# Optimization experiments

Measured on AMD Instinct MI355X. Metric: run time of the kernel, lower is better.

The kernel has to match this reference:

```python
import jax, jax.numpy as jnp
import numpy as np

DIM, H, KV, HD, WIN = 1024, 16, 4, 64, 512
EPS = 1e-6


def rmsnorm(x, w, eps=EPS):
    # torch.nn.RMSNorm: x * rsqrt(mean(x^2, -1) + eps) * w
    return x * jax.lax.rsqrt(jnp.mean(x * x, axis=-1, keepdims=True) + eps) * w


def setup_inputs() -> dict:
    key = jax.random.key(0)
    ks = jax.random.split(key, 7)
    B, T = 4, 2048
    s = 0.02
    return {
        "x": jax.random.normal(ks[0], (B, T, DIM), dtype=jnp.float32),
        "wq": jax.random.normal(ks[1], (H * HD, DIM), dtype=jnp.float32) * s,
        "wk": jax.random.normal(ks[2], (KV * HD, DIM), dtype=jnp.float32) * s,
        "wv": jax.random.normal(ks[3], (KV * HD, DIM), dtype=jnp.float32) * s,
        "wo": jax.random.normal(ks[4], (DIM, H * HD), dtype=jnp.float32) * s,
        "q_norm_w": jnp.ones((HD,), dtype=jnp.float32),
        "k_norm_w": jnp.ones((HD,), dtype=jnp.float32),
    }


def reference(x, wq, wk, wv, wo, q_norm_w, k_norm_w):
    B, T, D = x.shape
    rep = H // KV
    q = (x @ wq.T).reshape(B, T, H, HD)
    k = (x @ wk.T).reshape(B, T, KV, HD)
    v = (x @ wv.T).reshape(B, T, KV, HD)
    q = rmsnorm(q, q_norm_w)
    k = rmsnorm(k, k_norm_w)
    # GQA repeat: each kv head repeated `rep` times contiguously
    k = jnp.repeat(k, rep, axis=2)  # [B,T,H,HD]
    v = jnp.repeat(v, rep, axis=2)
    # scores [B,H,T,T]
    scores = jnp.einsum('bqhd,bkhd->bhqk', q, k) / jnp.sqrt(jnp.float32(HD))
    i = jnp.arange(T)[:, None]
    j = jnp.arange(T)[None, :]
    mask = (i >= j) & (i - j < WIN)  # causal sliding window band
    scores = jnp.where(mask, scores, -jnp.inf)
    attn = jax.nn.softmax(scores, axis=-1)
    y = jnp.einsum('bhqk,bkhd->bqhd', attn, v).reshape(B, T, H * HD)
    return y @ wo.T
```

## Files before the change

### kernel.cpp

```cpp
#include <hip/hip_runtime.h>
#include <hip/hip_bf16.h>

#define DIMD 1024
#define NH   16
#define NKV  4
#define HDIM 64
#define WINSZ 512
#define BB   4
#define TT   2048
#define MROWS (BB*TT)
#define NQKV 1536

typedef __attribute__((ext_vector_type(8))) short short8;
typedef __attribute__((ext_vector_type(4))) float f32x4;

static __device__ __forceinline__ short f2bf(float f) {
  __hip_bfloat16 h = __float2bfloat16(f);
  return __builtin_bit_cast(short, h);
}
static __device__ __forceinline__ float bf2f(short s) {
  return __bfloat162float(__builtin_bit_cast(__hip_bfloat16, s));
}
static __device__ __forceinline__ unsigned pk2(float a, float b) {
  unsigned lo = (unsigned short)f2bf(a);
  unsigned hi = (unsigned short)f2bf(b);
  return lo | (hi << 16);
}

static __device__ __forceinline__ void gld_lds16(const void* g, void* l) {
  __builtin_amdgcn_global_load_lds(
      (const __attribute__((address_space(1))) unsigned int*)g,
      (__attribute__((address_space(3))) unsigned int*)l, 16, 0, 0);
}

template<int N>
static __device__ __forceinline__ float dpp_ror(float x) {
  return __builtin_bit_cast(float, __builtin_amdgcn_update_dpp(
      0, __builtin_bit_cast(int, x), 0x120 + N, 0xF, 0xF, true));
}

__global__ __launch_bounds__(256) void cvt_all_kernel(
    const float* __restrict__ x, const float* __restrict__ wq,
    const float* __restrict__ wk, const float* __restrict__ wv,
    const float* __restrict__ wo,
    short* __restrict__ xb, short* __restrict__ wqkvb, short* __restrict__ wob) {
  size_t u = (size_t)blockIdx.x * 256 + threadIdx.x;
  const float* src; short* dst;
  if (u < 2097152)                   { src = x;  dst = xb; }
  else if ((u -= 2097152) < 262144)  { src = wq; dst = wqkvb; }
  else if ((u -= 262144) < 65536)    { src = wk; dst = wqkvb + 1024*1024; }
  else if ((u -= 65536) < 65536)     { src = wv; dst = wqkvb + 1280*1024; }
  else { u -= 65536;                   src = wo; dst = wob; }
  float4 v = ((const float4*)src)[u];
  short4 o;
  o.x = f2bf(v.x); o.y = f2bf(v.y); o.z = f2bf(v.z); o.w = f2bf(v.w);
  ((short4*)dst)[u] = o;
}

#define BMT 128
#define BNT 128
#define BKT 64

template<bool OUT_BF16>
__global__ __launch_bounds__(256) void gemm_bt(
    const short* __restrict__ A, const short* __restrict__ Bw,
    void* __restrict__ Cout, int M, int N, int K) {
  __shared__ __align__(16) short As[BMT*BKT];
  __shared__ __align__(16) short Bs[BNT*BKT];

  int nwg  = gridDim.x;
  int orig = blockIdx.x;
  int wg   = (orig & 7) * (nwg >> 3) + (orig >> 3);
  int tiles_n = N / BNT;
  int m0 = (wg / tiles_n) * BMT;
  int n0 = (wg % tiles_n) * BNT;

  int tid = threadIdx.x;
  int lane = tid & 63, wv = tid >> 6;
  int l15 = lane & 15, lg = lane >> 4;
  int wr = wv >> 1, wc = wv & 1;

  f32x4 acc[4][4] = {};

  for (int k0 = 0; k0 < K; k0 += BKT) {
    __syncthreads();
    const char* Abase = (const char*)(A + (size_t)m0 * K + k0);
    const char* Bbase = (const char*)(Bw + (size_t)n0 * K + k0);
#pragma unroll
    for (int i = 0; i < 4; ++i) {
      int idx = i * 256 + tid;
      int row = idx >> 3;
      int cb  = (idx & 7) << 4;
      int scb = cb ^ ((row & 7) << 4);
      gld_lds16(Abase + (size_t)row * (K * 2) + scb,
                (char*)As + ((i * 256 + wv * 64) << 4));
      gld_lds16(Bbase + (size_t)row * (K * 2) + scb,
                (char*)Bs + ((i * 256 + wv * 64) << 4));
    }
    __syncthreads();

#pragma unroll
    for (int kk = 0; kk < 2; ++kk) {
      short8 af[4], bfr[4];
      int kb = (kk * 32 + lg * 8) * 2;
#pragma unroll
      for (int mi = 0; mi < 4; ++mi) {
        int row = wr * 64 + mi * 16 + l15;
        af[mi] = *(const short8*)((const char*)As + row * 128 + (kb ^ ((row & 7) << 4)));
      }
#pragma unroll
      for (int ni = 0; ni < 4; ++ni) {
        int row = wc * 64 + ni * 16 + l15;
        bfr[ni] = *(const short8*)((const char*)Bs + row * 128 + (kb ^ ((row & 7) << 4)));
      }
#pragma unroll
      for (int mi = 0; mi < 4; ++mi)
#pragma unroll
        for (int ni = 0; ni < 4; ++ni)
          acc[mi][ni] = __builtin_amdgcn_mfma_f32_16x16x32_bf16(af[mi], bfr[ni], acc[mi][ni], 0, 0, 0);
    }
  }

  int crow0 = m0 + wr * 64, ccol0 = n0 + wc * 64;
#pragma unroll
  for (int mi = 0; mi < 4; ++mi)
#pragma unroll
    for (int ni = 0; ni < 4; ++ni)
#pragma unroll
      for (int r = 0; r < 4; ++r) {
        int row = crow0 + mi * 16 + lg * 4 + r;
        int col = ccol0 + ni * 16 + l15;
        float v = acc[mi][ni][r];
        if (OUT_BF16) ((short*)Cout)[(size_t)row * N + col] = f2bf(v);
        else          ((float*)Cout)[(size_t)row * N + col] = v;
      }
}

__global__ __launch_bounds__(256) void qk_norm_kernel(
    const short* __restrict__ qkv, const float* __restrict__ qw,
    const float* __restrict__ kw, short* __restrict__ Qh, short* __restrict__ Kh) {
  unsigned gid = blockIdx.x * 16u + (threadIdx.x >> 4);
  int l = threadIdx.x & 15;
  unsigned row = gid / 20u;
  int s = (int)(gid - row * 20u);
  int b = row >> 11, t = row & 2047;
  bool isq = s < 16;
  int col = isq ? s * 64 : 1024 + (s - 16) * 64;
  const short* rp = qkv + (size_t)row * NQKV + col + l * 4;
  short4 v4 = *(const short4*)rp;
  float f0 = bf2f(v4.x), f1 = bf2f(v4.y), f2 = bf2f(v4.z), f3 = bf2f(v4.w);
  float ss = f0 * f0 + f1 * f1 + f2 * f2 + f3 * f3;
  ss += dpp_ror<1>(ss); ss += dpp_ror<2>(ss);
  ss += dpp_ror<4>(ss); ss += dpp_ror<8>(ss);
  float r = rsqrtf(ss * (1.0f / 64.0f) + 1e-6f);
  float4 w4 = *(const float4*)((isq ? qw : kw) + l * 4);
  short4 o;
  o.x = f2bf(f0 * r * w4.x); o.y = f2bf(f1 * r * w4.y);
  o.z = f2bf(f2 * r * w4.z); o.w = f2bf(f3 * r * w4.w);
  if (isq) *(short4*)(Qh + (((size_t)b * NH + s) * TT + t) * HDIM + l * 4) = o;
  else     *(short4*)(Kh + (((size_t)b * NKV + (s - 16)) * TT + t) * HDIM + l * 4) = o;
}

__global__ __launch_bounds__(256) void vtrans_kernel(
    const short* __restrict__ qkv, short* __restrict__ Vt) {
  int tb = blockIdx.x, kv = blockIdx.y, b = blockIdx.z;
  __shared__ short tile[64][72];
  int tid = threadIdx.x;
#pragma unroll
  for (int i = 0; i < 2; ++i) {
    int idx = i * 256 + tid;
    int tr = idx >> 3;
    int c8 = (idx & 7) * 8;
    int t = tb * 64 + tr;
    const short* src = qkv + (size_t)(b * TT + t) * NQKV + 1280 + kv * 64 + c8;
    short8 v = *(const short8*)src;
#pragma unroll
    for (int j = 0; j < 8; ++j) tile[tr][c8 + j] = v[j];
  }
  __syncthreads();
#pragma unroll
  for (int i = 0; i < 2; ++i) {
    int idx = i * 256 + tid;
    int d = idx >> 3;
    int t8 = (idx & 7) * 8;
    short8 o;
#pragma unroll
    for (int j = 0; j < 8; ++j) o[j] = tile[t8 + j][d];
    short* dst = Vt + (((size_t)(b * NKV + kv) * HDIM) + d) * TT + tb * 64 + t8;
    *(short8*)dst = o;
  }
}

#define C1A 0.180336880f
#define C2A 11.5415603f

__global__ __launch_bounds__(128) void attn_kernel(
    const short* __restrict__ Qh, const short* __restrict__ Kh,
    const short* __restrict__ Vt, short* __restrict__ Y) {
  int wgid = blockIdx.x;
  int qh = wgid >> 6;
  int hb = wgid & 63;
  int h = hb >> 2, b = hb & 3;
  int tid = threadIdx.x, lane = tid & 63;
  int khalf = tid >> 6;
  int l15 = lane & 15, lg = lane >> 4;
  int kvh = h >> 2;
  int q0 = qh * 32;
  const short* Qp = Qh + (((size_t)b * NH + h) * TT + q0) * HDIM;
  const short* Kp = Kh + ((size_t)b * NKV + kvh) * TT * HDIM;
  const short* Vp = Vt + ((size_t)b * NKV + kvh) * HDIM * TT;

  short8 aqA0 = *(const short8*)(Qp + l15 * HDIM + lg * 8);
  short8 aqA1 = *(const short8*)(Qp + l15 * HDIM + 32 + lg * 8);
  short8 aqB0 = *(const short8*)(Qp + (16 + l15) * HDIM + lg * 8);
  short8 aqB1 = *(const short8*)(Qp + (16 + l15) * HDIM + 32 + lg * 8);

  float lpA = 0.f, lpB = 0.f;
  f32x4 yA[4] = {}, yB[4] = {};

  __shared__ __align__(16) char smem[9216];
  short* PA = (short*)smem + khalf * 2304;
  short* PB = PA + 1152;

  int lo = q0 - (WINSZ - 1); if (lo < 0) lo = 0;
  int klo = lo & ~63;
  int nt = (q0 + 32 - klo + 63) >> 6;
  int tmid = (nt + 1) >> 1;
  int t0 = khalf ? tmid : 0;
  int t1 = khalf ? nt : tmid;

  int qiA = q0 + l15, qiB = qiA + 16;

  for (int t = t0; t < t1; ++t) {
    int kc = klo + t * 64;
    short8 bk0[4], bk1[4], bv0[4], bv1[4];
#pragma unroll
    for (int nc = 0; nc < 4; ++nc) {
      const short* kb = Kp + (size_t)(kc + nc * 16 + l15) * HDIM + lg * 8;
      bk0[nc] = *(const short8*)kb;
      bk1[nc] = *(const short8*)(kb + 32);
    }
#pragma unroll
    for (int dt = 0; dt < 4; ++dt) {
      const short* vb = Vp + (size_t)(dt * 16 + l15) * TT + kc + lg * 8;
      bv0[dt] = *(const short8*)vb;
      bv1[dt] = *(const short8*)(vb + 32);
    }
    f32x4 sA[4], sB[4];
#pragma unroll
    for (int nc = 0; nc < 4; ++nc) {
      f32x4 zA = {}, zB = {};
      zA = __builtin_amdgcn_mfma_f32_16x16x32_bf16(bk0[nc], aqA0, zA, 0, 0, 0);
      zB = __builtin_amdgcn_mfma_f32_16x16x32_bf16(bk0[nc], aqB0, zB, 0, 0, 0);
      zA = __builtin_amdgcn_mfma_f32_16x16x32_bf16(bk1[nc], aqA1, zA, 0, 0, 0);
      zB = __builtin_amdgcn_mfma_f32_16x16x32_bf16(bk1[nc], aqB1, zB, 0, 0, 0);
      sA[nc] = zA; sB[nc] = zB;
    }
    bool intA = (kc >= q0 - 496) && (kc + 63 <= q0);
    bool intB = (kc >= q0 - 480) && (kc + 63 <= q0 + 16);
    if (intA && intB) {
#pragma unroll
      for (int nc = 0; nc < 4; ++nc) {
        float pa0 = __builtin_amdgcn_exp2f(fmaf(sA[nc][0], C1A, -C2A));
        float pa1 = __builtin_amdgcn_exp2f(fmaf(sA[nc][1], C1A, -C2A));
        float pa2 = __builtin_amdgcn_exp2f(fmaf(sA[nc][2], C1A, -C2A));
        float pa3 = __builtin_amdgcn_exp2f(fmaf(sA[nc][3], C1A, -C2A));
        float pb0 = __builtin_amdgcn_exp2f(fmaf(sB[nc][0], C1A, -C2A));
        float pb1 = __builtin_amdgcn_exp2f(fmaf(sB[nc][1], C1A, -C2A));
        float pb2 = __builtin_amdgcn_exp2f(fmaf(sB[nc][2], C1A, -C2A));
        float pb3 = __builtin_amdgcn_exp2f(fmaf(sB[nc][3], C1A, -C2A));
        lpA += (pa0 + pa1) + (pa2 + pa3);
        lpB += (pb0 + pb1) + (pb2 + pb3);
        *(uint2*)(PA + l15 * 72 + nc * 16 + lg * 4) = uint2{pk2(pa0, pa1), pk2(pa2, pa3)};
        *(uint2*)(PB + l15 * 72 + nc * 16 + lg * 4) = uint2{pk2(pb0, pb1), pk2(pb2, pb3)};
      }
    } else {
      int kjb = kc + lg * 4;
#pragma unroll
      for (int nc = 0; nc < 4; ++nc) {
        float pa[4], pb[4];
#pragma unroll
        for (int r = 0; r < 4; ++r) {
          int kj = kjb + nc * 16 + r;
          bool okA = (kj <= qiA) && (qiA - kj < WINSZ);
          bool okB = (kj <= qiB) && (qiB - kj < WINSZ);
          pa[r] = okA ? __builtin_amdgcn_exp2f(fmaf(sA[nc][r], C1A, -C2A)) : 0.f;
          pb[r] = okB ? __builtin_amdgcn_exp2f(fmaf(sB[nc][r], C1A, -C2A)) : 0.f;
        }
        lpA += (pa[0] + pa[1]) + (pa[2] + pa[3]);
        lpB += (pb[0] + pb[1]) + (pb[2] + pb[3]);
        *(uint2*)(PA + l15 * 72 + nc * 16 + lg * 4) = uint2{pk2(pa[0], pa[1]), pk2(pa[2], pa[3])};
        *(uint2*)(PB + l15 * 72 + nc * 16 + lg * 4) = uint2{pk2(pb[0], pb[1]), pk2(pb[2], pb[3])};
      }
    }
    short8 apA0 = *(const short8*)(PA + l15 * 72 + lg * 8);
    short8 apA1 = *(const short8*)(PA + l15 * 72 + 32 + lg * 8);
    short8 apB0 = *(const short8*)(PB + l15 * 72 + lg * 8);
    short8 apB1 = *(const short8*)(PB + l15 * 72 + 32 + lg * 8);
#pragma unroll
    for (int dt = 0; dt < 4; ++dt) {
      yA[dt] = __builtin_amdgcn_mfma_f32_16x16x32_bf16(apA0, bv0[dt], yA[dt], 0, 0, 0);
      yB[dt] = __builtin_amdgcn_mfma_f32_16x16x32_bf16(apB0, bv0[dt], yB[dt], 0, 0, 0);
      yA[dt] = __builtin_amdgcn_mfma_f32_16x16x32_bf16(apA1, bv1[dt], yA[dt], 0, 0, 0);
      yB[dt] = __builtin_amdgcn_mfma_f32_16x16x32_bf16(apB1, bv1[dt], yB[dt], 0, 0, 0);
    }
  }

  lpA += __shfl_xor(lpA, 16); lpA += __shfl_xor(lpA, 32);
  lpB += __shfl_xor(lpB, 16); lpB += __shfl_xor(lpB, 32);

  __syncthreads();
  f32x4* ybuf = (f32x4*)smem;
  float* lbufA = (float*)(smem + 8192);
  float* lbufB = lbufA + 16;
  if (khalf) {
#pragma unroll
    for (int dt = 0; dt < 4; ++dt) {
      ybuf[dt * 64 + lane] = yA[dt];
      ybuf[(4 + dt) * 64 + lane] = yB[dt];
    }
    if (lg == 0) { lbufA[l15] = lpA; lbufB[l15] = lpB; }
  }
  __syncthreads();
  if (!khalf) {
#pragma unroll
    for (int dt = 0; dt < 4; ++dt) {
      f32x4 pa = ybuf[dt * 64 + lane];
      f32x4 pb = ybuf[(4 + dt) * 64 + lane];
#pragma unroll
      for (int r = 0; r < 4; ++r) { yA[dt][r] += pa[r]; yB[dt][r] += pb[r]; }
    }
    float invqA = 1.0f / (lpA + lbufA[l15]);
    float invqB = 1.0f / (lpB + lbufB[l15]);
#pragma unroll
    for (int r = 0; r < 4; ++r) {
      float invA = __builtin_bit_cast(float, __builtin_amdgcn_ds_bpermute(
          (lg * 4 + r) << 2, __builtin_bit_cast(int, invqA)));
      float invB = __builtin_bit_cast(float, __builtin_amdgcn_ds_bpermute(
          (lg * 4 + r) << 2, __builtin_bit_cast(int, invqB)));
      int qiAo = q0 + lg * 4 + r, qiBo = qiAo + 16;
#pragma unroll
      for (int dt = 0; dt < 4; ++dt) {
        Y[((size_t)(b * TT + qiAo)) * DIMD + h * HDIM + dt * 16 + l15] = f2bf(yA[dt][r] * invA);
        Y[((size_t)(b * TT + qiBo)) * DIMD + h * HDIM + dt * 16 + l15] = f2bf(yB[dt][r] * invB);
      }
    }
  }
}

extern "C" void kernel_launch(void* const* d_in, const int* in_sizes, int n_in,
                              void* d_out, int out_size, void* d_ws, size_t ws_size,
                              hipStream_t stream) {
  const float* x  = (const float*)d_in[0];
  const float* wq = (const float*)d_in[1];
  const float* wk = (const float*)d_in[2];
  const float* wv = (const float*)d_in[3];
  const float* wo = (const float*)d_in[4];
  const float* qw = (const float*)d_in[5];
  const float* kw = (const float*)d_in[6];

  char* ws = (char*)d_ws;
  short* xb    = (short*)(ws + 0);
  short* wqkvb = (short*)(ws + 16777216);
  short* wob   = (short*)(ws + 19922944);
  short* qkv   = (short*)(ws + 22020096);
  short* Qh    = (short*)(ws + 47185920);
  short* Kh    = (short*)(ws + 63963136);
  short* Vt    = (short*)(ws + 68157440);
  short* Y     = xb;
  float* outp  = (float*)d_out;

  cvt_all_kernel<<<10752, 256, 0, stream>>>(x, wq, wk, wv, wo, xb, wqkvb, wob);
  gemm_bt<true><<<dim3(64 * 12), 256, 0, stream>>>(xb, wqkvb, (void*)qkv, MROWS, NQKV, DIMD);
  qk_norm_kernel<<<10240, 256, 0, stream>>>(qkv, qw, kw, Qh, Kh);
  vtrans_kernel<<<dim3(32, 4, 4), 256, 0, stream>>>(qkv, Vt);
  attn_kernel<<<4096, 128, 0, stream>>>(Qh, Kh, Vt, Y);
  gemm_bt<false><<<dim3(64 * 8), 256, 0, stream>>>(Y, wob, (void*)outp, MROWS, DIMD, DIMD);
}
```

Baseline: 146.4 us.

## Fuse QK RMSNorm into QKV GEMM epilogue and double-buffer K loads in attention

The QKV GEMM epilogue now computes the per-head RMSNorm for Q and K directly from fp32 accumulators. It writes head-major Qh/Kh plus a compact V buffer, which removes the separate qk_norm kernel and the full bf16 qkv intermediate round-trip. The attention loop is restructured to prefetch the next K tile into registers while the current tile is processed. The cost is higher register pressure in both kernels and scattered 2-byte epilogue stores. Normalization also now runs on unrounded fp32 values, which slightly changes numerics.

```diff
diff --git a/kernel.cpp b/kernel.cpp
--- a/kernel.cpp
+++ b/kernel.cpp
@@ -61,10 +61,11 @@
 #define BNT 128
 #define BKT 64
 
-template<bool OUT_BF16>
-__global__ __launch_bounds__(256) void gemm_bt(
+__global__ __launch_bounds__(256) void gemm_qkv(
     const short* __restrict__ A, const short* __restrict__ Bw,
-    void* __restrict__ Cout, int M, int N, int K) {
+    const float* __restrict__ qw, const float* __restrict__ kw,
+    short* __restrict__ Qh, short* __restrict__ Kh, short* __restrict__ Vbuf) {
+  const int M = MROWS, N = NQKV, K = DIMD;
   __shared__ __align__(16) short As[BMT*BKT];
   __shared__ __align__(16) short Bs[BNT*BKT];
 
@@ -122,6 +123,106 @@
   }
 
   int crow0 = m0 + wr * 64, ccol0 = n0 + wc * 64;
+  int s = ccol0 >> 6;
+  if (s < 20) {
+    const float* wptr = (s < 16) ? qw : kw;
+    float wl0 = wptr[l15],      wl1 = wptr[16 + l15];
+    float wl2 = wptr[32 + l15], wl3 = wptr[48 + l15];
+    short* hout = (s < 16) ? Qh : Kh;
+    int hidx = (s < 16) ? s : (s - 16);
+    int nheads = (s < 16) ? NH : NKV;
+#pragma unroll
+    for (int mi = 0; mi < 4; ++mi)
+#pragma unroll
+      for (int r = 0; r < 4; ++r) {
+        float a0 = acc[mi][0][r], a1 = acc[mi][1][r];
+        float a2 = acc[mi][2][r], a3 = acc[mi][3][r];
+        float ssq = a0 * a0 + a1 * a1 + a2 * a2 + a3 * a3;
+        ssq += dpp_ror<1>(ssq); ssq += dpp_ror<2>(ssq);
+        ssq += dpp_ror<4>(ssq); ssq += dpp_ror<8>(ssq);
+        float rn = rsqrtf(ssq * (1.0f / 64.0f) + 1e-6f);
+        int trow = crow0 + mi * 16 + lg * 4 + r;
+        int b = trow >> 11, tt = trow & 2047;
+        short* op = hout + (((size_t)b * nheads + hidx) * TT + tt) * HDIM;
+        op[l15]      = f2bf(a0 * rn * wl0);
+        op[16 + l15] = f2bf(a1 * rn * wl1);
+        op[32 + l15] = f2bf(a2 * rn * wl2);
+        op[48 + l15] = f2bf(a3 * rn * wl3);
+      }
+  } else {
+    int vc0 = ccol0 - 1280;
+#pragma unroll
+    for (int mi = 0; mi < 4; ++mi)
+#pragma unroll
+      for (int ni = 0; ni < 4; ++ni)
+#pragma unroll
+        for (int r = 0; r < 4; ++r) {
+          int trow = crow0 + mi * 16 + lg * 4 + r;
+          Vbuf[(size_t)trow * 256 + vc0 + ni * 16 + l15] = f2bf(acc[mi][ni][r]);
+        }
+  }
+}
+
+__global__ __launch_bounds__(256) void gemm_out(
+    const short* __restrict__ A, const short* __restrict__ Bw,
+    float* __restrict__ Cout, int M, int N, int K) {
+  __shared__ __align__(16) short As[BMT*BKT];
+  __shared__ __align__(16) short Bs[BNT*BKT];
+
+  int nwg  = gridDim.x;
+  int orig = blockIdx.x;
+  int wg   = (orig & 7) * (nwg >> 3) + (orig >> 3);
+  int tiles_n = N / BNT;
+  int m0 = (wg / tiles_n) * BMT;
+  int n0 = (wg % tiles_n) * BNT;
+
+  int tid = threadIdx.x;
+  int lane = tid & 63, wv = tid >> 6;
+  int l15 = lane & 15, lg = lane >> 4;
+  int wr = wv >> 1, wc = wv & 1;
+
+  f32x4 acc[4][4] = {};
+
+  for (int k0 = 0; k0 < K; k0 += BKT) {
+    __syncthreads();
+    const char* Abase = (const char*)(A + (size_t)m0 * K + k0);
+    const char* Bbase = (const char*)(Bw + (size_t)n0 * K + k0);
+#pragma unroll
+    for (int i = 0; i < 4; ++i) {
+      int idx = i * 256 + tid;
+      int row = idx >> 3;
+      int cb  = (idx & 7) << 4;
+      int scb = cb ^ ((row & 7) << 4);
+      gld_lds16(Abase + (size_t)row * (K * 2) + scb,
+                (char*)As + ((i * 256 + wv * 64) << 4));
+      gld_lds16(Bbase + (size_t)row * (K * 2) + scb,
+                (char*)Bs + ((i * 256 + wv * 64) << 4));
+    }
+    __syncthreads();
+
+#pragma unroll
+    for (int kk = 0; kk < 2; ++kk) {
+      short8 af[4], bfr[4];
+      int kb = (kk * 32 + lg * 8) * 2;
+#pragma unroll
+      for (int mi = 0; mi < 4; ++mi) {
+        int row = wr * 64 + mi * 16 + l15;
+        af[mi] = *(const short8*)((const char*)As + row * 128 + (kb ^ ((row & 7) << 4)));
+      }
+#pragma unroll
+      for (int ni = 0; ni < 4; ++ni) {
+        int row = wc * 64 + ni * 16 + l15;
+        bfr[ni] = *(const short8*)((const char*)Bs + row * 128 + (kb ^ ((row & 7) << 4)));
+      }
+#pragma unroll
+      for (int mi = 0; mi < 4; ++mi)
+#pragma unroll
+        for (int ni = 0; ni < 4; ++ni)
+          acc[mi][ni] = __builtin_amdgcn_mfma_f32_16x16x32_bf16(af[mi], bfr[ni], acc[mi][ni], 0, 0, 0);
+    }
+  }
+
+  int crow0 = m0 + wr * 64, ccol0 = n0 + wc * 64;
 #pragma unroll
   for (int mi = 0; mi < 4; ++mi)
 #pragma unroll
@@ -130,39 +231,12 @@
       for (int r = 0; r < 4; ++r) {
         int row = crow0 + mi * 16 + lg * 4 + r;
         int col = ccol0 + ni * 16 + l15;
-        float v = acc[mi][ni][r];
-        if (OUT_BF16) ((short*)Cout)[(size_t)row * N + col] = f2bf(v);
-        else          ((float*)Cout)[(size_t)row * N + col] = v;
-      }
-}
-
-__global__ __launch_bounds__(256) void qk_norm_kernel(
-    const short* __restrict__ qkv, const float* __restrict__ qw,
-    const float* __restrict__ kw, short* __restrict__ Qh, short* __restrict__ Kh) {
-  unsigned gid = blockIdx.x * 16u + (threadIdx.x >> 4);
-  int l = threadIdx.x & 15;
-  unsigned row = gid / 20u;
-  int s = (int)(gid - row * 20u);
-  int b = row >> 11, t = row & 2047;
-  bool isq = s < 16;
-  int col = isq ? s * 64 : 1024 + (s - 16) * 64;
-  const short* rp = qkv + (size_t)row * NQKV + col + l * 4;
-  short4 v4 = *(const short4*)rp;
-  float f0 = bf2f(v4.x), f1 = bf2f(v4.y), f2 = bf2f(v4.z), f3 = bf2f(v4.w);
-  float ss = f0 * f0 + f1 * f1 + f2 * f2 + f3 * f3;
-  ss += dpp_ror<1>(ss); ss += dpp_ror<2>(ss);
-  ss += dpp_ror<4>(ss); ss += dpp_ror<8>(ss);
-  float r = rsqrtf(ss * (1.0f / 64.0f) + 1e-6f);
-  float4 w4 = *(const float4*)((isq ? qw : kw) + l * 4);
-  short4 o;
-  o.x = f2bf(f0 * r * w4.x); o.y = f2bf(f1 * r * w4.y);
-  o.z = f2bf(f2 * r * w4.z); o.w = f2bf(f3 * r * w4.w);
-  if (isq) *(short4*)(Qh + (((size_t)b * NH + s) * TT + t) * HDIM + l * 4) = o;
-  else     *(short4*)(Kh + (((size_t)b * NKV + (s - 16)) * TT + t) * HDIM + l * 4) = o;
+        Cout[(size_t)row * N + col] = acc[mi][ni][r];
+      }
 }
 
 __global__ __launch_bounds__(256) void vtrans_kernel(
-    const short* __restrict__ qkv, short* __restrict__ Vt) {
+    const short* __restrict__ Vbuf, short* __restrict__ Vt) {
   int tb = blockIdx.x, kv = blockIdx.y, b = blockIdx.z;
   __shared__ short tile[64][72];
   int tid = threadIdx.x;
@@ -172,7 +246,7 @@
     int tr = idx >> 3;
     int c8 = (idx & 7) * 8;
     int t = tb * 64 + tr;
-    const short* src = qkv + (size_t)(b * TT + t) * NQKV + 1280 + kv * 64 + c8;
+    const short* src = Vbuf + (size_t)(b * TT + t) * 256 + kv * 64 + c8;
     short8 v = *(const short8*)src;
 #pragma unroll
     for (int j = 0; j < 8; ++j) tile[tr][c8 + j] = v[j];
@@ -231,15 +305,17 @@
 
   int qiA = q0 + l15, qiB = qiA + 16;
 
-  for (int t = t0; t < t1; ++t) {
-    int kc = klo + t * 64;
-    short8 bk0[4], bk1[4], bv0[4], bv1[4];
+  auto LOADK = [&](int kc, short8 (&bk0)[4], short8 (&bk1)[4]) {
 #pragma unroll
     for (int nc = 0; nc < 4; ++nc) {
       const short* kb = Kp + (size_t)(kc + nc * 16 + l15) * HDIM + lg * 8;
       bk0[nc] = *(const short8*)kb;
       bk1[nc] = *(const short8*)(kb + 32);
     }
+  };
+
+  auto PROC = [&](int kc, short8 (&bk0)[4], short8 (&bk1)[4]) {
+    short8 bv0[4], bv1[4];
 #pragma unroll
     for (int dt = 0; dt < 4; ++dt) {
       const short* vb = Vp + (size_t)(dt * 16 + l15) * TT + kc + lg * 8;
@@ -304,6 +380,17 @@
       yA[dt] = __builtin_amdgcn_mfma_f32_16x16x32_bf16(apA1, bv1[dt], yA[dt], 0, 0, 0);
       yB[dt] = __builtin_amdgcn_mfma_f32_16x16x32_bf16(apB1, bv1[dt], yB[dt], 0, 0, 0);
     }
+  };
+
+  short8 kA0[4], kA1[4], kB0[4], kB1[4];
+  int kc = klo + t0 * 64;
+  if (t0 < t1) LOADK(kc, kA0, kA1);
+  for (int t = t0; t < t1; t += 2) {
+    if (t + 1 < t1) LOADK(kc + 64, kB0, kB1);
+    PROC(kc, kA0, kA1);
+    if (t + 2 < t1) LOADK(kc + 128, kA0, kA1);
+    if (t + 1 < t1) PROC(kc + 64, kB0, kB1);
+    kc += 128;
   }
 
   lpA += __shfl_xor(lpA, 16); lpA += __shfl_xor(lpA, 32);
@@ -363,17 +450,16 @@
   short* xb    = (short*)(ws + 0);
   short* wqkvb = (short*)(ws + 16777216);
   short* wob   = (short*)(ws + 19922944);
-  short* qkv   = (short*)(ws + 22020096);
-  short* Qh    = (short*)(ws + 47185920);
-  short* Kh    = (short*)(ws + 63963136);
-  short* Vt    = (short*)(ws + 68157440);
+  short* Vbuf  = (short*)(ws + 22020096);
+  short* Qh    = (short*)(ws + 26214400);
+  short* Kh    = (short*)(ws + 42991616);
+  short* Vt    = (short*)(ws + 47185920);
   short* Y     = xb;
   float* outp  = (float*)d_out;
 
   cvt_all_kernel<<<10752, 256, 0, stream>>>(x, wq, wk, wv, wo, xb, wqkvb, wob);
-  gemm_bt<true><<<dim3(64 * 12), 256, 0, stream>>>(xb, wqkvb, (void*)qkv, MROWS, NQKV, DIMD);
-  qk_norm_kernel<<<10240, 256, 0, stream>>>(qkv, qw, kw, Qh, Kh);
-  vtrans_kernel<<<dim3(32, 4, 4), 256, 0, stream>>>(qkv, Vt);
+  gemm_qkv<<<768, 256, 0, stream>>>(xb, wqkvb, qw, kw, Qh, Kh, Vbuf);
+  vtrans_kernel<<<dim3(32, 4, 4), 256, 0, stream>>>(Vbuf, Vt);
   attn_kernel<<<4096, 128, 0, stream>>>(Qh, Kh, Vt, Y);
-  gemm_bt<false><<<dim3(64 * 8), 256, 0, stream>>>(Y, wob, (void*)outp, MROWS, DIMD, DIMD);
-}
+  gemm_out<<<512, 256, 0, stream>>>(Y, wob, outp, MROWS, DIMD, DIMD);
+}
```

New measurement: 155.1 us. +6.0%, slower.

## Split attention key range across four waves and raise MFMA priority

Applied to the files above, without the earlier changes.

The attention kernel now uses 256 threads per block, so four waves split the key tiles of each 32-query block instead of two, and their partial outputs and softmax denominators are reduced through shared memory. s_setprio is raised around the MFMA sections so matrix work is scheduled ahead of other waves. This shortens each block's serial loop and raises parallelism, at the cost of more shared memory per block, a larger cross-wave reduction and possibly fewer resident blocks.

```diff
diff --git a/kernel.cpp b/kernel.cpp
--- a/kernel.cpp
+++ b/kernel.cpp
@@ -194,7 +194,7 @@
 #define C1A 0.180336880f
 #define C2A 11.5415603f
 
-__global__ __launch_bounds__(128) void attn_kernel(
+__global__ __launch_bounds__(256) void attn_kernel(
     const short* __restrict__ Qh, const short* __restrict__ Kh,
     const short* __restrict__ Vt, short* __restrict__ Y) {
   int wgid = blockIdx.x;
@@ -202,7 +202,7 @@
   int hb = wgid & 63;
   int h = hb >> 2, b = hb & 3;
   int tid = threadIdx.x, lane = tid & 63;
-  int khalf = tid >> 6;
+  int wq4 = tid >> 6;
   int l15 = lane & 15, lg = lane >> 4;
   int kvh = h >> 2;
   int q0 = qh * 32;
@@ -218,16 +218,15 @@
   float lpA = 0.f, lpB = 0.f;
   f32x4 yA[4] = {}, yB[4] = {};
 
-  __shared__ __align__(16) char smem[9216];
-  short* PA = (short*)smem + khalf * 2304;
+  __shared__ __align__(16) char smem[25088];
+  short* PA = (short*)smem + wq4 * 2304;
   short* PB = PA + 1152;
 
   int lo = q0 - (WINSZ - 1); if (lo < 0) lo = 0;
   int klo = lo & ~63;
   int nt = (q0 + 32 - klo + 63) >> 6;
-  int tmid = (nt + 1) >> 1;
-  int t0 = khalf ? tmid : 0;
-  int t1 = khalf ? nt : tmid;
+  int t0 = (wq4 * nt) >> 2;
+  int t1 = ((wq4 + 1) * nt) >> 2;
 
   int qiA = q0 + l15, qiB = qiA + 16;
 
@@ -247,6 +246,7 @@
       bv1[dt] = *(const short8*)(vb + 32);
     }
     f32x4 sA[4], sB[4];
+    __builtin_amdgcn_s_setprio(1);
 #pragma unroll
     for (int nc = 0; nc < 4; ++nc) {
       f32x4 zA = {}, zB = {};
@@ -256,6 +256,7 @@
       zB = __builtin_amdgcn_mfma_f32_16x16x32_bf16(bk1[nc], aqB1, zB, 0, 0, 0);
       sA[nc] = zA; sB[nc] = zB;
     }
+    __builtin_amdgcn_s_setprio(0);
     bool intA = (kc >= q0 - 496) && (kc + 63 <= q0);
     bool intB = (kc >= q0 - 480) && (kc + 63 <= q0 + 16);
     if (intA && intB) {
@@ -297,6 +298,7 @@
     short8 apA1 = *(const short8*)(PA + l15 * 72 + 32 + lg * 8);
     short8 apB0 = *(const short8*)(PB + l15 * 72 + lg * 8);
     short8 apB1 = *(const short8*)(PB + l15 * 72 + 32 + lg * 8);
+    __builtin_amdgcn_s_setprio(1);
 #pragma unroll
     for (int dt = 0; dt < 4; ++dt) {
       yA[dt] = __builtin_amdgcn_mfma_f32_16x16x32_bf16(apA0, bv0[dt], yA[dt], 0, 0, 0);
@@ -304,6 +306,7 @@
       yA[dt] = __builtin_amdgcn_mfma_f32_16x16x32_bf16(apA1, bv1[dt], yA[dt], 0, 0, 0);
       yB[dt] = __builtin_amdgcn_mfma_f32_16x16x32_bf16(apB1, bv1[dt], yB[dt], 0, 0, 0);
     }
+    __builtin_amdgcn_s_setprio(0);
   }
 
   lpA += __shfl_xor(lpA, 16); lpA += __shfl_xor(lpA, 32);
@@ -311,27 +314,35 @@
 
   __syncthreads();
   f32x4* ybuf = (f32x4*)smem;
-  float* lbufA = (float*)(smem + 8192);
-  float* lbufB = lbufA + 16;
-  if (khalf) {
+  float* lbuf = (float*)(smem + 24576);
+  if (wq4) {
+    int wb = (wq4 - 1) * 512;
 #pragma unroll
     for (int dt = 0; dt < 4; ++dt) {
-      ybuf[dt * 64 + lane] = yA[dt];
-      ybuf[(4 + dt) * 64 + lane] = yB[dt];
-    }
-    if (lg == 0) { lbufA[l15] = lpA; lbufB[l15] = lpB; }
+      ybuf[wb + dt * 64 + lane] = yA[dt];
+      ybuf[wb + (4 + dt) * 64 + lane] = yB[dt];
+    }
+    if (lg == 0) {
+      lbuf[(wq4 - 1) * 32 + l15] = lpA;
+      lbuf[(wq4 - 1) * 32 + 16 + l15] = lpB;
+    }
   }
   __syncthreads();
-  if (!khalf) {
-#pragma unroll
-    for (int dt = 0; dt < 4; ++dt) {
-      f32x4 pa = ybuf[dt * 64 + lane];
-      f32x4 pb = ybuf[(4 + dt) * 64 + lane];
-#pragma unroll
-      for (int r = 0; r < 4; ++r) { yA[dt][r] += pa[r]; yB[dt][r] += pb[r]; }
-    }
-    float invqA = 1.0f / (lpA + lbufA[l15]);
-    float invqB = 1.0f / (lpB + lbufB[l15]);
+  if (wq4 == 0) {
+#pragma unroll
+    for (int w = 0; w < 3; ++w) {
+#pragma unroll
+      for (int dt = 0; dt < 4; ++dt) {
+        f32x4 pa = ybuf[w * 512 + dt * 64 + lane];
+        f32x4 pb = ybuf[w * 512 + (4 + dt) * 64 + lane];
+#pragma unroll
+        for (int r = 0; r < 4; ++r) { yA[dt][r] += pa[r]; yB[dt][r] += pb[r]; }
+      }
+      lpA += lbuf[w * 32 + l15];
+      lpB += lbuf[w * 32 + 16 + l15];
+    }
+    float invqA = 1.0f / lpA;
+    float invqB = 1.0f / lpB;
 #pragma unroll
     for (int r = 0; r < 4; ++r) {
       float invA = __builtin_bit_cast(float, __builtin_amdgcn_ds_bpermute(
@@ -374,6 +385,6 @@
   gemm_bt<true><<<dim3(64 * 12), 256, 0, stream>>>(xb, wqkvb, (void*)qkv, MROWS, NQKV, DIMD);
   qk_norm_kernel<<<10240, 256, 0, stream>>>(qkv, qw, kw, Qh, Kh);
   vtrans_kernel<<<dim3(32, 4, 4), 256, 0, stream>>>(qkv, Vt);
-  attn_kernel<<<4096, 128, 0, stream>>>(Qh, Kh, Vt, Y);
+  attn_kernel<<<4096, 256, 0, stream>>>(Qh, Kh, Vt, Y);
   gemm_bt<false><<<dim3(64 * 8), 256, 0, stream>>>(Y, wob, (void*)outp, MROWS, DIMD, DIMD);
 }
```

New measurement: 151.9 us. +3.8%, slower.
